# Performance work log

Hardware: AMD Instinct MI355X
Metric: run time of the kernel (lower is better)

Reference implementation:

```python
import jax, jax.numpy as jnp
import numpy as np

EPS = 1e-5
K = 20

def knn_idx(x, k):
    # x: (B, N, C). Torch computes -||xi-xj||^2 and takes topk (largest => nearest).
    xx = jnp.sum(x * x, axis=-1)                      # (B, N)
    inner = jnp.einsum('bnc,bmc->bnm', x, x)          # (B, N, N)
    neg_dist = 2.0 * inner - xx[:, :, None] - xx[:, None, :]
    return jax.lax.top_k(neg_dist, k)[1]              # (B, N, k) int32

def edge_feature(x, k):
    # x: (B, N, C) -> (B, N, k, 2C) = concat(neighbor - center, center)
    B = x.shape[0]
    idx = knn_idx(x, k)
    nb = x[jnp.arange(B)[:, None, None], idx]         # (B, N, k, C) gather
    ctr = jnp.broadcast_to(x[:, :, None, :], nb.shape)
    return jnp.concatenate([nb - ctr, ctr], axis=-1)

def batchnorm(x, gamma, beta, axes):
    # training-mode BN over `axes` (per-channel on last axis)
    m = jnp.mean(x, axis=axes, keepdims=True)
    v = jnp.var(x, axis=axes, keepdims=True)
    return (x - m) * jax.lax.rsqrt(v + EPS) * gamma + beta

def lrelu(x):
    return jnp.where(x >= 0, x, 0.2 * x)

def conv_bn_act(x, w, g, b):
    # 1x1 conv on (B, N, k, Cin) with weight (Cout, Cin), BN over (B, N, k)
    y = jnp.einsum('bnkc,oc->bnko', x, w)
    return lrelu(batchnorm(y, g, b, (0, 1, 2)))


def setup_inputs() -> dict:
    key = jax.random.key(0)
    ks = jax.random.split(key, 16)
    B, N = 4, 4096
    d = {'x': jax.random.normal(ks[0], (B, 3, N), dtype=jnp.float32)}
    d['w1'] = jax.random.normal(ks[1], (64, 6),    dtype=jnp.float32) * 0.1
    d['w2'] = jax.random.normal(ks[2], (64, 64),   dtype=jnp.float32) * 0.1
    d['w3'] = jax.random.normal(ks[3], (64, 128),  dtype=jnp.float32) * 0.1
    d['w4'] = jax.random.normal(ks[4], (64, 64),   dtype=jnp.float32) * 0.1
    d['w5'] = jax.random.normal(ks[5], (64, 128),  dtype=jnp.float32) * 0.1
    d['w6'] = jax.random.normal(ks[6], (1024, 192), dtype=jnp.float32) * 0.05
    d['wl'] = jax.random.normal(ks[7], (512, 1024), dtype=jnp.float32) * 0.05
    for i, c in zip(range(1, 8), [64, 64, 64, 64, 64, 1024, 512]):
        d[f'g{i}'] = jnp.ones((c,), jnp.float32)
        d[f'b{i}'] = jnp.zeros((c,), jnp.float32)
    return d


def reference(x, w1, w2, w3, w4, w5, w6, wl,
              g1, b1, g2, b2, g3, b3, g4, b4, g5, b5, g6, b6, g7, b7):
    p = jnp.transpose(x[:, :3, :], (0, 2, 1))         # (B, N, 3)
    # EdgeConv block 1
    e = edge_feature(p, K)                            # (B, N, k, 6)
    h = conv_bn_act(e, w1, g1, b1)
    h = conv_bn_act(h, w2, g2, b2)
    x1 = jnp.max(h, axis=2)                           # (B, N, 64)
    # EdgeConv block 2
    e = edge_feature(x1, K)                           # (B, N, k, 128)
    h = conv_bn_act(e, w3, g3, b3)
    h = conv_bn_act(h, w4, g4, b4)
    x2 = jnp.max(h, axis=2)
    # EdgeConv block 3
    e = edge_feature(x2, K)
    h = conv_bn_act(e, w5, g5, b5)
    x3 = jnp.max(h, axis=2)
    # point-wise 1x1 conv to 1024 then global max pool
    cat = jnp.concatenate([x1, x2, x3], axis=-1)      # (B, N, 192)
    h = lrelu(batchnorm(jnp.einsum('bnc,oc->bno', cat, w6), g6, b6, (0, 1)))
    g = jnp.max(h, axis=1)                            # (B, 1024)
    out = batchnorm(g @ wl.T, g7, b7, (0,))           # (B, 512)
    return out
```

## Files before the change

### kernel.cpp

```cpp
#include <hip/hip_runtime.h>

static constexpr int PB  = 4;
static constexpr int PN  = 4096;
static constexpr int PK  = 20;
static constexpr int PNT = PB*PN*PK;
#define NEGF (-3.402823466e38f)

__device__ __forceinline__ float lrelu_f(float x){ return x >= 0.f ? x : 0.2f*x; }

__device__ __forceinline__ unsigned int ordf(float v){
  unsigned int u = __float_as_uint(v);
  unsigned int mask = ((unsigned int)(((int)u) >> 31)) | 0x80000000u;
  return u ^ mask;
}

#define FMA4C(accv, av, bv) { accv = fmaf((av).x,(bv).x,accv); accv = fmaf((av).y,(bv).y,accv); \
                              accv = fmaf((av).z,(bv).z,accv); accv = fmaf((av).w,(bv).w,accv); }

__global__ __launch_bounds__(512) void k_knn3(const float* __restrict__ x, int* __restrict__ idxb){
  __shared__ float4 pts[PN];
  int t = threadIdx.x;
  int b = blockIdx.y;
  const float* xb = x + (size_t)b*3*PN;
  for(int i=t;i<PN;i+=512){
    float a0 = xb[i], a1 = xb[PN+i], a2 = xb[2*PN+i];
    float s = a0*a0; s = fmaf(a1,a1,s); s = fmaf(a2,a2,s);
    pts[i] = make_float4(a0,a1,a2,s);
  }
  __syncthreads();
  int lane = t & 63, w = t >> 6;
  int row = blockIdx.x*8 + w;
  float4 pi = pts[row];
  unsigned long long removed = 0ull;

#define KDIST(E) ({ float4 pj_ = pts[lane + ((E)<<6)]; \
    float dt_ = pi.x*pj_.x; dt_ = fmaf(pi.y,pj_.y,dt_); dt_ = fmaf(pi.z,pj_.z,dt_); \
    fmaf(2.f,dt_,-pi.w) - pj_.w; })

  float gv0,gv1,gv2,gv3,gv4,gv5,gv6,gv7;
  int   gi0,gi1,gi2,gi3,gi4,gi5,gi6,gi7;
#define KBUILDG(G) { float gm_=NEGF; int ge_=(G)*8; \
    _Pragma("unroll") for(int e_=(G)*8; e_<(G)*8+8; e_++){ \
      bool ok_ = ((removed >> e_) & 1ull) == 0ull; \
      float d_ = KDIST(e_); \
      bool bt_ = ok_ && (d_ > gm_); gm_ = bt_ ? d_ : gm_; ge_ = bt_ ? e_ : ge_; } \
    gv##G = gm_; gi##G = ge_; }
  KBUILDG(0) KBUILDG(1) KBUILDG(2) KBUILDG(3) KBUILDG(4) KBUILDG(5) KBUILDG(6) KBUILDG(7)

  float lmax; int le;
#define KLBEST { lmax = gv0; le = gi0; \
    if(gv1>lmax){lmax=gv1;le=gi1;} if(gv2>lmax){lmax=gv2;le=gi2;} \
    if(gv3>lmax){lmax=gv3;le=gi3;} if(gv4>lmax){lmax=gv4;le=gi4;} \
    if(gv5>lmax){lmax=gv5;le=gi5;} if(gv6>lmax){lmax=gv6;le=gi6;} \
    if(gv7>lmax){lmax=gv7;le=gi7;} }
  KLBEST

  int myidx = 0;
  for(int k=0;k<PK;k++){
    unsigned long long key = ((unsigned long long)ordf(lmax) << 32) |
                             (unsigned int)(~(lane + (le<<6)));
    #pragma unroll
    for(int s=1;s<64;s<<=1){
      unsigned long long o = __shfl_xor(key, s);
      if(o > key) key = o;
    }
    int jw = (int)(~((unsigned int)key));
    if(lane == k) myidx = jw;
    if((jw & 63) == lane){
      int e = jw >> 6;
      removed |= (1ull << e);
      int q = e >> 3;
      if(q==0){ KBUILDG(0) } else if(q==1){ KBUILDG(1) }
      else if(q==2){ KBUILDG(2) } else if(q==3){ KBUILDG(3) }
      else if(q==4){ KBUILDG(4) } else if(q==5){ KBUILDG(5) }
      else if(q==6){ KBUILDG(6) } else { KBUILDG(7) }
      KLBEST
    }
  }
  if(lane < PK) idxb[((size_t)b*PN + row)*PK + lane] = myidx;
#undef KDIST
#undef KBUILDG
#undef KLBEST
}

__global__ __launch_bounds__(256) void k_dist64(const float* __restrict__ Xb, const float* __restrict__ xxb,
                                                float* __restrict__ D){
  __shared__ float Xi[128*32];
  __shared__ float Xj[128*32];
  __shared__ float xxi[128], xxj[128];
  int t = threadIdx.x;
  int p = blockIdx.x;
  int bi = (int)((65.0f - sqrtf(4225.0f - 8.0f*(float)p)) * 0.5f);
  while((bi+1)*32 - ((bi+1)*bi)/2 <= p) bi++;
  while(bi*32 - (bi*(bi-1))/2 > p) bi--;
  int bj = bi + (p - (bi*32 - (bi*(bi-1))/2));
  int i0 = bi*128, j0 = bj*128;
  int prg = t>>4, cq = t&15;
  float acc[8][8];
  #pragma unroll
  for(int pp=0;pp<8;pp++)
    #pragma unroll
    for(int oc=0;oc<8;oc++) acc[pp][oc] = 0.f;

  for(int h=0;h<2;h++){
    if(h) __syncthreads();
    #pragma unroll
    for(int k=0;k<4;k++){
      int fid = t + k*256; int row = fid>>3, c4 = fid&7;
      ((float4*)Xi)[row*8 + (c4^(row&7))] = ((const float4*)(Xb + (size_t)(i0+row)*64 + h*32))[c4];
      ((float4*)Xj)[row*8 + (c4^(row&7))] = ((const float4*)(Xb + (size_t)(j0+row)*64 + h*32))[c4];
    }
    if(h==0){
      if(t < 128) xxi[t] = xxb[i0+t];
      else        xxj[t-128] = xxb[j0+t-128];
    }
    __syncthreads();
    #pragma unroll 4
    for(int c4=0;c4<8;c4++){
      float4 a[8], bb[8];
      #pragma unroll
      for(int pp=0;pp<8;pp++){ int row = prg*8+pp; a[pp] = ((const float4*)Xi)[row*8 + (c4^(row&7))]; }
      #pragma unroll
      for(int oc=0;oc<8;oc++){ int col = cq+16*oc;  bb[oc] = ((const float4*)Xj)[col*8 + (c4^(col&7))]; }
      #pragma unroll
      for(int pp=0;pp<8;pp++)
        #pragma unroll
        for(int oc=0;oc<8;oc++) FMA4C(acc[pp][oc], a[pp], bb[oc]);
    }
  }
  #pragma unroll
  for(int pp=0;pp<8;pp++){
    int r = prg*8+pp;
    float xi2 = xxi[r];
    float* Drow = D + (size_t)(i0+r)*PN + j0;
    #pragma unroll
    for(int oc=0;oc<8;oc++){
      int c = cq + 16*oc;
      Drow[c] = fmaf(2.f, acc[pp][oc], -xi2) - xxj[c];
    }
  }
  if(bi != bj){
    #pragma unroll
    for(int oc=0;oc<8;oc++){
      int c = cq + 16*oc;
      float xj2 = xxj[c];
      float* Dcol = D + (size_t)(j0+c)*PN + i0 + prg*8;
      float4 t0, t1;
      t0.x = fmaf(2.f, acc[0][oc], -xj2) - xxi[prg*8+0];
      t0.y = fmaf(2.f, acc[1][oc], -xj2) - xxi[prg*8+1];
      t0.z = fmaf(2.f, acc[2][oc], -xj2) - xxi[prg*8+2];
      t0.w = fmaf(2.f, acc[3][oc], -xj2) - xxi[prg*8+3];
      t1.x = fmaf(2.f, acc[4][oc], -xj2) - xxi[prg*8+4];
      t1.y = fmaf(2.f, acc[5][oc], -xj2) - xxi[prg*8+5];
      t1.z = fmaf(2.f, acc[6][oc], -xj2) - xxi[prg*8+6];
      t1.w = fmaf(2.f, acc[7][oc], -xj2) - xxi[prg*8+7];
      ((float4*)Dcol)[0] = t0;
      ((float4*)Dcol)[1] = t1;
    }
  }
}

__global__ __launch_bounds__(256) void k_topk(const float* __restrict__ D, int* __restrict__ idxb){
  int t = threadIdx.x, lane = t & 63, w = t >> 6;
  int row = blockIdx.x*4 + w;
  const float4* rp = (const float4*)(D + (size_t)row*PN + lane*64);
  float v[64];
  #pragma unroll
  for(int c=0;c<16;c++){
    float4 q = rp[c];
    v[4*c+0]=q.x; v[4*c+1]=q.y; v[4*c+2]=q.z; v[4*c+3]=q.w;
  }
  float gv0,gv1,gv2,gv3,gv4,gv5,gv6,gv7;
  int   gi0,gi1,gi2,gi3,gi4,gi5,gi6,gi7;
#define TBUILDG(G) { float gm_=NEGF; int ge_=(G)*8; \
    _Pragma("unroll") for(int e_=(G)*8; e_<(G)*8+8; e_++){ \
      bool bt_ = v[e_] > gm_; gm_ = bt_ ? v[e_] : gm_; ge_ = bt_ ? e_ : ge_; } \
    gv##G = gm_; gi##G = ge_; }
#define TPOIS(G) { _Pragma("unroll") for(int e_=(G)*8; e_<(G)*8+8; e_++){ \
      if(e_ == rel) v[e_] = NEGF; } }
  TBUILDG(0) TBUILDG(1) TBUILDG(2) TBUILDG(3) TBUILDG(4) TBUILDG(5) TBUILDG(6) TBUILDG(7)
  float lmax; int li;
#define TLBEST { lmax = gv0; li = gi0; \
    if(gv1>lmax){lmax=gv1;li=gi1;} if(gv2>lmax){lmax=gv2;li=gi2;} \
    if(gv3>lmax){lmax=gv3;li=gi3;} if(gv4>lmax){lmax=gv4;li=gi4;} \
    if(gv5>lmax){lmax=gv5;li=gi5;} if(gv6>lmax){lmax=gv6;li=gi6;} \
    if(gv7>lmax){lmax=gv7;li=gi7;} }
  TLBEST
  int myidx = 0;
  for(int k=0;k<PK;k++){
    float g = lmax;
    #pragma unroll
    for(int s=32;s>=1;s>>=1) g = fmaxf(g, __shfl_xor(g, s));
    unsigned long long mask = __ballot(lmax == g);
    int wl = __ffsll((unsigned long long)mask) - 1;
    int rel = __shfl(li, wl);
    if(lane == k) myidx = wl*64 + rel;
    if(lane == wl){
      int q = rel >> 3;
      if(q==0){ TPOIS(0) TBUILDG(0) } else if(q==1){ TPOIS(1) TBUILDG(1) }
      else if(q==2){ TPOIS(2) TBUILDG(2) } else if(q==3){ TPOIS(3) TBUILDG(3) }
      else if(q==4){ TPOIS(4) TBUILDG(4) } else if(q==5){ TPOIS(5) TBUILDG(5) }
      else if(q==6){ TPOIS(6) TBUILDG(6) } else { TPOIS(7) TBUILDG(7) }
      TLBEST
    }
  }
  if(lane < PK) idxb[row*PK + lane] = myidx;
#undef TBUILDG
#undef TPOIS
#undef TLBEST
}

__global__ __launch_bounds__(256) void k_nodeUV3(const float* __restrict__ x, const float* __restrict__ w1,
                                                 float* __restrict__ U, float* __restrict__ V){
  __shared__ float ww[384];
  int t = threadIdx.x;
  for(int k=t;k<384;k+=256) ww[k] = w1[k];
  __syncthreads();
  int g = blockIdx.x*256 + t;
  int ng = g >> 6, o = g & 63;
  int b = ng >> 12, n = ng & 4095;
  const float* xb = x + (size_t)b*3*PN;
  float p0 = xb[n], p1 = xb[PN+n], p2 = xb[2*PN+n];
  const float* wr = ww + o*6;
  float u = p0*wr[0]; u = fmaf(p1,wr[1],u); u = fmaf(p2,wr[2],u);
  float vv = p0*(wr[3]-wr[0]); vv = fmaf(p1, wr[4]-wr[1], vv); vv = fmaf(p2, wr[5]-wr[2], vv);
  U[(size_t)ng*64+o] = u;
  V[(size_t)ng*64+o] = vv;
}

__global__ __launch_bounds__(256) void k_nodeUV64(const float* __restrict__ xf, const float* __restrict__ w,
                                                  float* __restrict__ U, float* __restrict__ V){
  __shared__ float xbuf[128*64];
  __shared__ float wbuf[128*64];
  int t = threadIdx.x;
  int r0 = blockIdx.x * 128;
  #pragma unroll
  for(int k=0;k<8;k++){
    int fid = t + k*256; int row = fid>>4, c4 = fid&15;
    ((float4*)xbuf)[row*16 + (c4^(row&15))] = ((const float4*)(xf + (size_t)(r0+row)*64))[c4];
    float4 wv;
    if(row < 64){
      wv = ((const float4*)(w + (size_t)row*128))[c4];
    } else {
      float4 w2v = ((const float4*)(w + (size_t)(row-64)*128 + 64))[c4];
      float4 w1v = ((const float4*)(w + (size_t)(row-64)*128))[c4];
      wv.x = w2v.x-w1v.x; wv.y = w2v.y-w1v.y; wv.z = w2v.z-w1v.z; wv.w = w2v.w-w1v.w;
    }
    ((float4*)wbuf)[row*16 + (c4^(row&15))] = wv;
  }
  __syncthreads();
  int rg = t>>4, cq = t&15;
  float acc[8][8];
  #pragma unroll
  for(int pp=0;pp<8;pp++)
    #pragma unroll
    for(int oc=0;oc<8;oc++) acc[pp][oc] = 0.f;
  #pragma unroll 4
  for(int c4=0;c4<16;c4++){
    float4 a[8], bb[8];
    #pragma unroll
    for(int pp=0;pp<8;pp++){ int row = rg*8+pp; a[pp] = ((const float4*)xbuf)[row*16 + (c4^(row&15))]; }
    #pragma unroll
    for(int oc=0;oc<8;oc++){ int col = cq+16*oc;  bb[oc] = ((const float4*)wbuf)[col*16 + (c4^(col&15))]; }
    #pragma unroll
    for(int pp=0;pp<8;pp++)
      #pragma unroll
      for(int oc=0;oc<8;oc++) FMA4C(acc[pp][oc], a[pp], bb[oc]);
  }
  #pragma unroll
  for(int pp=0;pp<8;pp++){
    int r = r0 + rg*8+pp;
    #pragma unroll
    for(int oc=0;oc<8;oc++){
      int col = cq + 16*oc;
      if(col < 64) U[(size_t)r*64 + col] = acc[pp][oc];
      else         V[(size_t)r*64 + col-64] = acc[pp][oc];
    }
  }
}

__global__ __launch_bounds__(256) void k_statUV(const float* __restrict__ U, const float* __restrict__ V,
                                                const int* __restrict__ idx, float* __restrict__ part){
  __shared__ float4 sArr[256];
  __shared__ float4 qArr[256];
  int t = threadIdx.x; int blk = blockIdx.x;
  int ch4 = t & 15, sub = t >> 4;
  int qbase = blk*640;
  float4 s = make_float4(0,0,0,0), qq = make_float4(0,0,0,0);
  for(int r=sub; r<640; r+=16){
    int q = qbase + r;
    int pt = q/PK;
    int b = pt >> 12;
    int j = idx[q];
    float4 u4 = ((const float4*)(U + (size_t)(b*PN+j)*64))[ch4];
    float4 v4 = ((const float4*)(V + (size_t)pt*64))[ch4];
    float4 y4;
    y4.x = u4.x+v4.x; y4.y = u4.y+v4.y; y4.z = u4.z+v4.z; y4.w = u4.w+v4.w;
    s.x += y4.x; s.y += y4.y; s.z += y4.z; s.w += y4.w;
    qq.x = fmaf(y4.x,y4.x,qq.x); qq.y = fmaf(y4.y,y4.y,qq.y);
    qq.z = fmaf(y4.z,y4.z,qq.z); qq.w = fmaf(y4.w,y4.w,qq.w);
  }
  sArr[t] = s; qArr[t] = qq;
  __syncthreads();
  if(t < 16){
    float4 S = make_float4(0,0,0,0), Q = make_float4(0,0,0,0);
    #pragma unroll
    for(int g=0;g<16;g++){
      float4 a = sArr[g*16 + t], b = qArr[g*16 + t];
      S.x+=a.x; S.y+=a.y; S.z+=a.z; S.w+=a.w;
      Q.x+=b.x; Q.y+=b.y; Q.z+=b.z; Q.w+=b.w;
    }
    ((float4*)(part + (size_t)blk*128))[t] = S;
    ((float4*)(part + (size_t)blk*128 + 64))[t] = Q;
  }
}

__global__ __launch_bounds__(256) void k_convAF(const float* __restrict__ U, const float* __restrict__ V,
                                                const int* __restrict__ idx, const float* __restrict__ wg,
                                                const float* __restrict__ sb, float* __restrict__ y,
                                                float* __restrict__ part){
  __shared__ float hbuf[128*64];
  __shared__ float wbuf[64*64];
  int t = threadIdx.x;
  int q0 = blockIdx.x * 128;
  #pragma unroll
  for(int k=0;k<8;k++){
    int fid = t + k*256; int row = fid>>4, c4 = fid&15;
    int q = q0 + row;
    int pt = q/PK; int b = pt>>12; int j = idx[q];
    float4 uu = ((const float4*)(U + (size_t)(b*PN+j)*64))[c4];
    float4 vv = ((const float4*)(V + (size_t)pt*64))[c4];
    float4 sc = ((const float4*)sb)[c4];
    float4 bi = ((const float4*)(sb+1024))[c4];
    float4 h;
    h.x = lrelu_f(fmaf(uu.x+vv.x, sc.x, bi.x));
    h.y = lrelu_f(fmaf(uu.y+vv.y, sc.y, bi.y));
    h.z = lrelu_f(fmaf(uu.z+vv.z, sc.z, bi.z));
    h.w = lrelu_f(fmaf(uu.w+vv.w, sc.w, bi.w));
    ((float4*)hbuf)[row*16 + (c4 ^ (row&15))] = h;
  }
  #pragma unroll
  for(int k=0;k<4;k++){
    int fid = t + k*256; int row = fid>>4, c4 = fid&15;
    ((float4*)wbuf)[row*16 + (c4 ^ (row&15))] = ((const float4*)(wg + row*64))[c4];
  }
  __syncthreads();
  int prg = t >> 4, cq = t & 15;
  float acc[8][4];
  #pragma unroll
  for(int pp=0;pp<8;pp++)
    #pragma unroll
    for(int oc=0;oc<4;oc++) acc[pp][oc] = 0.f;
  #pragma unroll 4
  for(int c4=0;c4<16;c4++){
    float4 a[8], b4[4];
    #pragma unroll
    for(int pp=0;pp<8;pp++){ int row = prg*8+pp; a[pp] = ((const float4*)hbuf)[row*16 + (c4^(row&15))]; }
    #pragma unroll
    for(int oc=0;oc<4;oc++){ int och = cq + 16*oc; b4[oc] = ((const float4*)wbuf)[och*16 + (c4^(och&15))]; }
    #pragma unroll
    for(int pp=0;pp<8;pp++)
      #pragma unroll
      for(int oc=0;oc<4;oc++) FMA4C(acc[pp][oc], a[pp], b4[oc]);
  }
  #pragma unroll
  for(int pp=0;pp<8;pp++)
    #pragma unroll
    for(int oc=0;oc<4;oc++)
      y[(size_t)(q0 + prg*8+pp)*64 + cq + 16*oc] = acc[pp][oc];

  float s_[4], q_[4];
  #pragma unroll
  for(int oc=0;oc<4;oc++){
    float s = 0.f, q = 0.f;
    #pragma unroll
    for(int pp=0;pp<8;pp++){ s += acc[pp][oc]; q = fmaf(acc[pp][oc], acc[pp][oc], q); }
    s_[oc] = s; q_[oc] = q;
  }
  __syncthreads();
  float* ls = wbuf;
  #pragma unroll
  for(int oc=0;oc<4;oc++){
    ls[(cq + 16*oc)*16 + prg]        = s_[oc];
    ls[2048 + (cq + 16*oc)*16 + prg] = q_[oc];
  }
  __syncthreads();
  if(t < 64){
    float S = 0.f, Q = 0.f;
    #pragma unroll
    for(int g=0;g<16;g++){ S += ls[t*16+g]; Q += ls[2048 + t*16+g]; }
    part[(size_t)blockIdx.x*128 + t] = S;
    part[(size_t)blockIdx.x*128 + 64 + t] = Q;
  }
}

__global__ __launch_bounds__(256) void k_red1024(const float* __restrict__ y6, float* __restrict__ part){
  int t = threadIdx.x; int blk = blockIdx.x;
  const float4* base = (const float4*)(y6 + (size_t)blk*128*1024);
  float4 s = make_float4(0,0,0,0), q = make_float4(0,0,0,0);
  for(int r=0;r<128;r++){
    float4 v = base[r*256 + t];
    s.x += v.x; s.y += v.y; s.z += v.z; s.w += v.w;
    q.x = fmaf(v.x,v.x,q.x); q.y = fmaf(v.y,v.y,q.y); q.z = fmaf(v.z,v.z,q.z); q.w = fmaf(v.w,v.w,q.w);
  }
  ((float4*)(part + (size_t)blk*2048))[t] = s;
  ((float4*)(part + (size_t)blk*2048 + 1024))[t] = q;
}

__global__ __launch_bounds__(256) void k_fin(const float* __restrict__ part, int nparts, int chn, float cnt,
                                             const float* __restrict__ gamma, const float* __restrict__ beta,
                                             float* __restrict__ sb){
  __shared__ float ls[512];
  int t = threadIdx.x;
  int chl = t & 15, sub = t >> 4;
  int ch = blockIdx.x*16 + chl;
  float S = 0.f, Q = 0.f;
  for(int p=sub; p<nparts; p+=16){
    S += part[(size_t)p*2*chn + ch];
    Q += part[(size_t)p*2*chn + chn + ch];
  }
  ls[t] = S; ls[256+t] = Q;
  __syncthreads();
  if(t < 16){
    float Sa = 0.f, Qa = 0.f;
    #pragma unroll
    for(int s=0;s<16;s++){ Sa += ls[s*16+t]; Qa += ls[256+s*16+t]; }
    int c = blockIdx.x*16 + t;
    float m  = Sa/cnt;
    float vr = Qa/cnt - m*m;
    float sc = gamma[c] * rsqrtf(vr + 1e-5f);
    sb[c] = sc; sb[1024+c] = beta[c] - m*sc;
  }
}

__global__ __launch_bounds__(256) void k_finish(const float* __restrict__ y, const float* __restrict__ sb,
                                                float* __restrict__ xo, float* __restrict__ xxo){
  __shared__ float ls[256];
  int t = threadIdx.x;
  int pt = blockIdx.x*16 + (t>>4), c4 = t&15;
  const float4* base = (const float4*)(y + (size_t)pt*20*64);
  float4 sc = ((const float4*)sb)[c4];
  float4 bi = ((const float4*)(sb+1024))[c4];
  float4 m = make_float4(NEGF,NEGF,NEGF,NEGF);
  #pragma unroll 4
  for(int k=0;k<20;k++){
    float4 v = base[k*16 + c4];
    v.x = lrelu_f(fmaf(v.x, sc.x, bi.x)); v.y = lrelu_f(fmaf(v.y, sc.y, bi.y));
    v.z = lrelu_f(fmaf(v.z, sc.z, bi.z)); v.w = lrelu_f(fmaf(v.w, sc.w, bi.w));
    m.x = fmaxf(m.x,v.x); m.y = fmaxf(m.y,v.y); m.z = fmaxf(m.z,v.z); m.w = fmaxf(m.w,v.w);
  }
  ((float4*)(xo + (size_t)pt*64))[c4] = m;
  float ss = m.x*m.x; ss = fmaf(m.y,m.y,ss); ss = fmaf(m.z,m.z,ss); ss = fmaf(m.w,m.w,ss);
  ls[t] = ss;
  __syncthreads();
  if(c4 == 0){
    float S = 0.f;
    #pragma unroll
    for(int c=0;c<16;c++) S += ls[(t & 0xF0) + c];
    xxo[pt] = S;
  }
}

__global__ __launch_bounds__(256) void k_finishUV(const float* __restrict__ U, const float* __restrict__ V,
                                                  const int* __restrict__ idx, const float* __restrict__ sb,
                                                  float* __restrict__ xo){
  int t = threadIdx.x;
  int pt = blockIdx.x*16 + (t>>4), c4 = t&15;
  int b = pt >> 12;
  float4 sc = ((const float4*)sb)[c4];
  float4 bi = ((const float4*)(sb+1024))[c4];
  float4 vv = ((const float4*)(V + (size_t)pt*64))[c4];
  float4 m = make_float4(NEGF,NEGF,NEGF,NEGF);
  const int* ip = idx + (size_t)pt*PK;
  #pragma unroll 4
  for(int k=0;k<PK;k++){
    int j = ip[k];
    float4 uu = ((const float4*)(U + (size_t)(b*PN+j)*64))[c4];
    float4 v;
    v.x = lrelu_f(fmaf(uu.x+vv.x, sc.x, bi.x)); v.y = lrelu_f(fmaf(uu.y+vv.y, sc.y, bi.y));
    v.z = lrelu_f(fmaf(uu.z+vv.z, sc.z, bi.z)); v.w = lrelu_f(fmaf(uu.w+vv.w, sc.w, bi.w));
    m.x = fmaxf(m.x,v.x); m.y = fmaxf(m.y,v.y); m.z = fmaxf(m.z,v.z); m.w = fmaxf(m.w,v.w);
  }
  ((float4*)(xo + (size_t)pt*64))[c4] = m;
}

__global__ __launch_bounds__(256) void k_gemm6(const float* __restrict__ x1, const float* __restrict__ x2,
                                               const float* __restrict__ x3, const float* __restrict__ w6,
                                               float* __restrict__ y6){
  __shared__ float cb[128*64];
  __shared__ float wb[64*64];
  int t = threadIdx.x;
  int rb = blockIdx.x >> 4;
  int ob = blockIdx.x & 15;
  size_t r0 = (size_t)rb*128; int o0 = ob*64;
  int prg = t >> 4, cq = t & 15;
  float acc[8][4];
  #pragma unroll
  for(int pp=0;pp<8;pp++)
    #pragma unroll
    for(int oc=0;oc<4;oc++) acc[pp][oc] = 0.f;
  const float* srcs[3] = {x1, x2, x3};
  for(int ph=0; ph<3; ph++){
    __syncthreads();
    const float* src = srcs[ph];
    #pragma unroll
    for(int k=0;k<8;k++){
      int fid = t + k*256; int row = fid>>4, c4 = fid&15;
      ((float4*)cb)[row*16 + (c4^(row&15))] = ((const float4*)(src + (r0+row)*64))[c4];
    }
    #pragma unroll
    for(int k=0;k<4;k++){
      int fid = t + k*256; int row = fid>>4, c4 = fid&15;
      ((float4*)wb)[row*16 + (c4^(row&15))] = ((const float4*)(w6 + (size_t)(o0+row)*192 + ph*64))[c4];
    }
    __syncthreads();
    #pragma unroll 4
    for(int c4=0;c4<16;c4++){
      float4 a[8], b4[4];
      #pragma unroll
      for(int pp=0;pp<8;pp++){ int row = prg*8+pp; a[pp] = ((const float4*)cb)[row*16 + (c4^(row&15))]; }
      #pragma unroll
      for(int oc=0;oc<4;oc++){ int och = cq + 16*oc; b4[oc] = ((const float4*)wb)[och*16 + (c4^(och&15))]; }
      #pragma unroll
      for(int pp=0;pp<8;pp++)
        #pragma unroll
        for(int oc=0;oc<4;oc++) FMA4C(acc[pp][oc], a[pp], b4[oc]);
    }
  }
  #pragma unroll
  for(int pp=0;pp<8;pp++)
    #pragma unroll
    for(int oc=0;oc<4;oc++)
      y6[(r0 + prg*8+pp)*1024 + o0 + cq + 16*oc] = acc[pp][oc];
}

__global__ __launch_bounds__(256) void k_gmax(const float* __restrict__ y6, const float* __restrict__ sb,
                                              float* __restrict__ gpart){
  int t = threadIdx.x; int blk = blockIdx.x;
  const float4* base = (const float4*)(y6 + (size_t)blk*256*1024);
  float4 sc = ((const float4*)sb)[t];
  float4 bi = ((const float4*)(sb+1024))[t];
  float4 m = make_float4(NEGF,NEGF,NEGF,NEGF);
  for(int r=0;r<256;r++){
    float4 v = base[r*256 + t];
    v.x = lrelu_f(fmaf(v.x, sc.x, bi.x)); v.y = lrelu_f(fmaf(v.y, sc.y, bi.y));
    v.z = lrelu_f(fmaf(v.z, sc.z, bi.z)); v.w = lrelu_f(fmaf(v.w, sc.w, bi.w));
    m.x = fmaxf(m.x,v.x); m.y = fmaxf(m.y,v.y); m.z = fmaxf(m.z,v.z); m.w = fmaxf(m.w,v.w);
  }
  ((float4*)(gpart + (size_t)blk*1024))[t] = m;
}

__global__ __launch_bounds__(256) void k_gmaxfin(const float* __restrict__ gpart, float* __restrict__ g){
  int b = blockIdx.x, t = threadIdx.x;
  float4 m = make_float4(NEGF,NEGF,NEGF,NEGF);
  for(int c=0;c<16;c++){
    float4 v = ((const float4*)(gpart + ((size_t)b*16 + c)*1024))[t];
    m.x = fmaxf(m.x,v.x); m.y = fmaxf(m.y,v.y); m.z = fmaxf(m.z,v.z); m.w = fmaxf(m.w,v.w);
  }
  ((float4*)(g + (size_t)b*1024))[t] = m;
}

__global__ __launch_bounds__(256) void k_final(const float* __restrict__ g, const float* __restrict__ wl,
                                               const float* __restrict__ g7, const float* __restrict__ b7,
                                               float* __restrict__ out){
  int gt = blockIdx.x*256 + threadIdx.x;
  int o = gt >> 2, b = gt & 3;
  const float4* gb = (const float4*)(g + (size_t)b*1024);
  const float4* wr = (const float4*)(wl + (size_t)o*1024);
  float acc = 0.f;
  #pragma unroll 4
  for(int c=0;c<256;c++){
    float4 a = gb[c], w = wr[c];
    acc = fmaf(a.x,w.x,acc); acc = fmaf(a.y,w.y,acc);
    acc = fmaf(a.z,w.z,acc); acc = fmaf(a.w,w.w,acc);
  }
  float s = acc + __shfl_xor(acc, 1);
  s = s + __shfl_xor(s, 2);
  float m = s * 0.25f;
  float d = acc - m;
  float vv = d*d;
  float v2 = vv + __shfl_xor(vv, 1);
  v2 = v2 + __shfl_xor(v2, 2);
  float var = v2 * 0.25f;
  out[b*512 + o] = d * rsqrtf(var + 1e-5f) * g7[o] + b7[o];
}

extern "C" void kernel_launch(void* const* d_in, const int* in_sizes, int n_in,
                              void* d_out, int out_size, void* d_ws, size_t ws_size,
                              hipStream_t stream){
  const float* x  = (const float*)d_in[0];
  const float* w1 = (const float*)d_in[1];
  const float* w2 = (const float*)d_in[2];
  const float* w3 = (const float*)d_in[3];
  const float* w4 = (const float*)d_in[4];
  const float* w5 = (const float*)d_in[5];
  const float* w6 = (const float*)d_in[6];
  const float* wl = (const float*)d_in[7];
  const float* g1 = (const float*)d_in[8];  const float* b1 = (const float*)d_in[9];
  const float* g2 = (const float*)d_in[10]; const float* b2 = (const float*)d_in[11];
  const float* g3 = (const float*)d_in[12]; const float* b3 = (const float*)d_in[13];
  const float* g4 = (const float*)d_in[14]; const float* b4 = (const float*)d_in[15];
  const float* g5 = (const float*)d_in[16]; const float* b5 = (const float*)d_in[17];
  const float* g6 = (const float*)d_in[18]; const float* b6 = (const float*)d_in[19];
  const float* g7 = (const float*)d_in[20]; const float* b7 = (const float*)d_in[21];
  float* out = (float*)d_out;

  float* ws    = (float*)d_ws;
  float* xx    = ws;
  int*   idx   = (int*)(ws + 16384);
  float* y     = ws + 344064;
  float* Dbuf  = y;
  float* x1    = ws + 21315584;
  float* x2    = x1 + 1048576;
  float* x3    = x2 + 1048576;
  float* part  = x3 + 1048576;
  float* sb    = part + 327680;
  float* gpart = sb + 2048;
  float* g     = gpart + 65536;
  float* U     = g + 4096;
  float* V     = U + 1048576;

  k_knn3<<<dim3(512,4),512,0,stream>>>(x, idx);
  k_nodeUV3<<<4096,256,0,stream>>>(x, w1, U, V);
  k_statUV<<<512,256,0,stream>>>(U, V, idx, part);
  k_fin<<<4,256,0,stream>>>(part, 512, 64, (float)PNT, g1, b1, sb);
  k_convAF<<<2560,256,0,stream>>>(U, V, idx, w2, sb, y, part);
  k_fin<<<4,256,0,stream>>>(part, 2560, 64, (float)PNT, g2, b2, sb);
  k_finish<<<1024,256,0,stream>>>(y, sb, x1, xx);

  for(int b=0;b<PB;b++){
    k_dist64<<<528,256,0,stream>>>(x1 + (size_t)b*PN*64, xx + b*PN, Dbuf);
    k_topk<<<1024,256,0,stream>>>(Dbuf, idx + (size_t)b*PN*PK);
  }
  k_nodeUV64<<<128,256,0,stream>>>(x1, w3, U, V);
  k_statUV<<<512,256,0,stream>>>(U, V, idx, part);
  k_fin<<<4,256,0,stream>>>(part, 512, 64, (float)PNT, g3, b3, sb);
  k_convAF<<<2560,256,0,stream>>>(U, V, idx, w4, sb, y, part);
  k_fin<<<4,256,0,stream>>>(part, 2560, 64, (float)PNT, g4, b4, sb);
  k_finish<<<1024,256,0,stream>>>(y, sb, x2, xx);

  for(int b=0;b<PB;b++){
    k_dist64<<<528,256,0,stream>>>(x2 + (size_t)b*PN*64, xx + b*PN, Dbuf);
    k_topk<<<1024,256,0,stream>>>(Dbuf, idx + (size_t)b*PN*PK);
  }
  k_nodeUV64<<<128,256,0,stream>>>(x2, w5, U, V);
  k_statUV<<<512,256,0,stream>>>(U, V, idx, part);
  k_fin<<<4,256,0,stream>>>(part, 512, 64, (float)PNT, g5, b5, sb);
  k_finishUV<<<1024,256,0,stream>>>(U, V, idx, sb, x3);

  k_gemm6<<<2048,256,0,stream>>>(x1, x2, x3, w6, y);
  k_red1024<<<128,256,0,stream>>>(y, part);
  k_fin<<<64,256,0,stream>>>(part, 128, 1024, 16384.f, g6, b6, sb);
  k_gmax<<<64,256,0,stream>>>(y, sb, gpart);
  k_gmaxfin<<<4,256,0,stream>>>(gpart, g);
  k_final<<<8,256,0,stream>>>(g, wl, g7, b7, out);
}
```

Baseline: 1.254 ms.

## Use float max-reduce for kNN argmax and widen gemm6 output tile

The kNN selection loop in k_knn3 now replaces the 64-bit packed-key shuffle reduction with a float fmax butterfly plus a ballot. The index comes from a single shuffle when the max is unique and from a second 32-bit min-reduction when there are ties. This cuts 64-bit shuffle traffic on the serial top-20 loop. Separately, k_gemm6 now computes 128 output channels per block instead of 64 (8x8 accumulators per thread, half the blocks), raising register pressure in exchange for more reuse of the staged point tile.

```diff
diff --git a/kernel.cpp b/kernel.cpp
--- a/kernel.cpp
+++ b/kernel.cpp
@@ -7,12 +7,6 @@
 #define NEGF (-3.402823466e38f)
 
 __device__ __forceinline__ float lrelu_f(float x){ return x >= 0.f ? x : 0.2f*x; }
-
-__device__ __forceinline__ unsigned int ordf(float v){
-  unsigned int u = __float_as_uint(v);
-  unsigned int mask = ((unsigned int)(((int)u) >> 31)) | 0x80000000u;
-  return u ^ mask;
-}
 
 #define FMA4C(accv, av, bv) { accv = fmaf((av).x,(bv).x,accv); accv = fmaf((av).y,(bv).y,accv); \
                               accv = fmaf((av).z,(bv).z,accv); accv = fmaf((av).w,(bv).w,accv); }
@@ -57,14 +51,21 @@
 
   int myidx = 0;
   for(int k=0;k<PK;k++){
-    unsigned long long key = ((unsigned long long)ordf(lmax) << 32) |
-                             (unsigned int)(~(lane + (le<<6)));
-    #pragma unroll
-    for(int s=1;s<64;s<<=1){
-      unsigned long long o = __shfl_xor(key, s);
-      if(o > key) key = o;
-    }
-    int jw = (int)(~((unsigned int)key));
+    float g = lmax;
+    #pragma unroll
+    for(int s=32;s>=1;s>>=1) g = fmaxf(g, __shfl_xor(g, s));
+    unsigned long long cand = __ballot(lmax == g);
+    int jw;
+    if(__popcll(cand) == 1){
+      int wl = __ffsll(cand) - 1;
+      int e  = __shfl(le, wl);
+      jw = wl + (e<<6);
+    } else {
+      unsigned jj = (lmax == g) ? (unsigned)(lane + (le<<6)) : 0xFFFFFFFFu;
+      #pragma unroll
+      for(int s=32;s>=1;s>>=1){ unsigned o = __shfl_xor(jj, s); jj = (o < jj) ? o : jj; }
+      jw = (int)jj;
+    }
     if(lane == k) myidx = jw;
     if((jw & 63) == lane){
       int e = jw >> 6;
@@ -488,17 +489,17 @@
                                                const float* __restrict__ x3, const float* __restrict__ w6,
                                                float* __restrict__ y6){
   __shared__ float cb[128*64];
-  __shared__ float wb[64*64];
-  int t = threadIdx.x;
-  int rb = blockIdx.x >> 4;
-  int ob = blockIdx.x & 15;
-  size_t r0 = (size_t)rb*128; int o0 = ob*64;
+  __shared__ float wb[128*64];
+  int t = threadIdx.x;
+  int rb = blockIdx.x >> 3;
+  int ob = blockIdx.x & 7;
+  size_t r0 = (size_t)rb*128; int o0 = ob*128;
   int prg = t >> 4, cq = t & 15;
-  float acc[8][4];
+  float acc[8][8];
   #pragma unroll
   for(int pp=0;pp<8;pp++)
     #pragma unroll
-    for(int oc=0;oc<4;oc++) acc[pp][oc] = 0.f;
+    for(int oc=0;oc<8;oc++) acc[pp][oc] = 0.f;
   const float* srcs[3] = {x1, x2, x3};
   for(int ph=0; ph<3; ph++){
     __syncthreads();
@@ -507,30 +508,26 @@
     for(int k=0;k<8;k++){
       int fid = t + k*256; int row = fid>>4, c4 = fid&15;
       ((float4*)cb)[row*16 + (c4^(row&15))] = ((const float4*)(src + (r0+row)*64))[c4];
-    }
-    #pragma unroll
-    for(int k=0;k<4;k++){
-      int fid = t + k*256; int row = fid>>4, c4 = fid&15;
       ((float4*)wb)[row*16 + (c4^(row&15))] = ((const float4*)(w6 + (size_t)(o0+row)*192 + ph*64))[c4];
     }
     __syncthreads();
     #pragma unroll 4
     for(int c4=0;c4<16;c4++){
-      float4 a[8], b4[4];
+      float4 a[8], b8[8];
       #pragma unroll
       for(int pp=0;pp<8;pp++){ int row = prg*8+pp; a[pp] = ((const float4*)cb)[row*16 + (c4^(row&15))]; }
       #pragma unroll
-      for(int oc=0;oc<4;oc++){ int och = cq + 16*oc; b4[oc] = ((const float4*)wb)[och*16 + (c4^(och&15))]; }
+      for(int oc=0;oc<8;oc++){ int och = cq + 16*oc; b8[oc] = ((const float4*)wb)[och*16 + (c4^(och&15))]; }
       #pragma unroll
       for(int pp=0;pp<8;pp++)
         #pragma unroll
-        for(int oc=0;oc<4;oc++) FMA4C(acc[pp][oc], a[pp], b4[oc]);
+        for(int oc=0;oc<8;oc++) FMA4C(acc[pp][oc], a[pp], b8[oc]);
     }
   }
   #pragma unroll
   for(int pp=0;pp<8;pp++)
     #pragma unroll
-    for(int oc=0;oc<4;oc++)
+    for(int oc=0;oc<8;oc++)
       y6[(r0 + prg*8+pp)*1024 + o0 + cq + 16*oc] = acc[pp][oc];
 }
 
@@ -648,7 +645,7 @@
   k_fin<<<4,256,0,stream>>>(part, 512, 64, (float)PNT, g5, b5, sb);
   k_finishUV<<<1024,256,0,stream>>>(U, V, idx, sb, x3);
 
-  k_gemm6<<<2048,256,0,stream>>>(x1, x2, x3, w6, y);
+  k_gemm6<<<1024,256,0,stream>>>(x1, x2, x3, w6, y);
   k_red1024<<<128,256,0,stream>>>(y, part);
   k_fin<<<64,256,0,stream>>>(part, 128, 1024, 16384.f, g6, b6, sb);
   k_gmax<<<64,256,0,stream>>>(y, sb, gpart);
```

After: 1.245 ms. No clear change (-0.7%).
